# Kernel tuning notes

Hardware: AMD Instinct MI355X
Metric: run time of the kernel (lower is better)

Reference implementation:

```python
import jax, jax.numpy as jnp
import numpy as np

EPS = 1e-07
N, Q = 1368, 21
WS = [16, 32, 64]
ST = [4, 8, 16]
OC = [64, 128, 256]


def _num_pos(n, w, s):
    return int((n - w) / s - EPS) + 1


def setup_inputs() -> dict:
    key = jax.random.key(0)
    kx, k0, k1, k2 = jax.random.split(key, 4)
    B = 64
    x = jax.random.normal(kx, (B, Q, N), dtype=jnp.float32)
    ws = []
    for kk, (w, s, d) in zip([k0, k1, k2], zip(WS, ST, OC)):
        P = _num_pos(N, w, s)
        # xavier-style small init, shape (Nk, q*w) as in FilterbankLinear.weight
        scale = np.sqrt(2.0 / (Q * w + d)).astype(np.float32)
        ws.append(scale * jax.random.normal(kk, (d * P, Q * w), dtype=jnp.float32))
    return {"x": x, "w0": ws[0], "w1": ws[1], "w2": ws[2]}


def _filterbank_linear(x, W, w, s, d):
    # x: (B, q, N); W: (d*P, q*w)
    B, q, n = x.shape
    P = _num_pos(n, w, s)
    # window starts: j*s for j in range(P-1), last window anchored at n-w
    starts = np.concatenate([np.arange(P - 1) * s, np.array([n - w])])
    idx = starts[:, None] + np.arange(w)            # (P, w) static gather indices
    win = x[:, :, idx]                              # (B, q, P, w)
    win = jnp.transpose(win, (0, 2, 1, 3)).reshape(B, P, q * w)  # (B, P, q*w), channel-major like fbank
    h = jnp.einsum('bpf,pdf->bpd', win, W.reshape(P, d, q * w))
    return h.reshape(B, P * d)


def reference(x, w0, w1, w2):
    # FilterbankEdge.forward(x, sample=False): concat of each FilterbankLinear output
    outs = [
        _filterbank_linear(x, W, w, s, d)
        for W, (w, s, d) in zip([w0, w1, w2], zip(WS, ST, OC))
    ]
    return jnp.concatenate(outs, axis=-1)  # (B, 64000)
```

## Files before the change

### kernel.cpp

```cpp
#include <hip/hip_runtime.h>

#define QDIM 21
#define NDIM 1368
#define QN (QDIM * NDIM)
#define OUTSTRIDE 64000
#define XTOT (64 * QN)

typedef __attribute__((ext_vector_type(4))) float f32x4;
typedef __attribute__((ext_vector_type(8))) short bf16x8s;
typedef __attribute__((ext_vector_type(4))) unsigned int u32x4;

typedef __attribute__((address_space(1))) const unsigned int* gas_p;
typedef __attribute__((address_space(3))) unsigned int* las_p;

static __device__ __forceinline__ void gload16(const void* g, char* l) {
    __builtin_amdgcn_global_load_lds((gas_p)g, (las_p)(void*)l, 16, 0, 0);
}

static __device__ __forceinline__ unsigned int pk2(float lo, float hi) {
    unsigned int a = __float_as_uint(lo) + 0x8000u;
    unsigned int b = __float_as_uint(hi) + 0x8000u;
    return __builtin_amdgcn_perm(b, a, 0x07060302);
}

static __device__ __forceinline__ bf16x8s pack8(f32x4 lo, f32x4 hi) {
    u32x4 p;
    p[0] = pk2(lo[0], lo[1]);
    p[1] = pk2(lo[2], lo[3]);
    p[2] = pk2(hi[0], hi[1]);
    p[3] = pk2(hi[2], hi[3]);
    return __builtin_bit_cast(bf16x8s, p);
}

static __device__ __forceinline__ int chunk_swz(int idx, int n) {
    int xcd = idx & 7;
    int i   = idx >> 3;
    int q = n >> 3, r = n & 7;
    int base = (xcd < r) ? xcd * (q + 1) : r * (q + 1) + (xcd - r) * q;
    return base + i;
}

__global__ __launch_bounds__(256)
void xcvt(const float* __restrict__ x, unsigned short* __restrict__ xb) {
    int i = (blockIdx.x * 256 + threadIdx.x) * 8;
    if (i >= XTOT) return;
    f32x4 lo = *(const f32x4*)(x + i);
    f32x4 hi = *(const f32x4*)(x + i + 4);
    *(u32x4*)(xb + i) = __builtin_bit_cast(u32x4, pack8(lo, hi));
}

template<int WLOG2, int NTX, int D, int P, int S, int K, bool ABF16>
__device__ __forceinline__ void fbk_body(const float* __restrict__ x,
                                         const unsigned short* __restrict__ xb,
                                         const float* __restrict__ W,
                                         float* __restrict__ out, int bid,
                                         char* ldsraw) {
    constexpr int WWIN = 1 << WLOG2;
    constexpr int G = (K + 31) / 32;
    constexpr bool TAIL = (K % 32) != 0;
    constexpr int KREM = K & 31;
    constexpr int FMAXC = (K - 4) & ~3;
    constexpr int ASTB = ABF16 ? 4096 : 8192;
    constexpr int STB  = ASTB + 8192;

    const int n0 = (bid % NTX) * 64;
    const int p  = bid / NTX;
    const int start = (p == P - 1) ? (NDIM - WWIN) : p * S;

    const int tid  = threadIdx.x;
    const int wid  = tid >> 6;
    const int lane = tid & 63;
    const int wm = (wid >> 1) * 32;
    const int wn = (wid & 1) * 32;
    const int lr = lane & 15;
    const int hi = lane >> 4;
    const int kb = hi * 8;

    const int lrow = lane >> 3;
    const int g4   = ((lane & 7) ^ lrow) * 4;
    const float* Wp  = W + (size_t)(p * D + n0) * K;
    const float* wb0 = Wp + (size_t)(16 * wid + lrow) * K;
    const float* wb1 = wb0 + (size_t)8 * K;
    const int wB = 2048 * wid;

    const unsigned short* xr0 = xb + (size_t)(16 * wid + (lane >> 2)) * QN + start;
    const float* xf0 = x + (size_t)(16 * wid + lrow) * QN + start;

    auto STAGE = [&](int t, int sbase) {
        if constexpr (ABF16) {
            int fa = t * 32 + (lane & 3) * 8;
            if constexpr (TAIL) fa = (fa > K - 8) ? (K - 8) : fa;
            int qa = fa >> WLOG2, ja = fa & (WWIN - 1);
            gload16(xr0 + qa * NDIM + ja, ldsraw + sbase + 1024 * wid);
        } else {
            int fa = t * 32 + g4;
            if constexpr (TAIL) fa = (fa > FMAXC) ? FMAXC : fa;
            int qa = fa >> WLOG2, ja = fa & (WWIN - 1);
            const float* ga = xf0 + qa * NDIM + ja;
            char* la = ldsraw + sbase + 2048 * wid;
            gload16(ga, la);
            gload16(ga + (size_t)8 * QN, la + 1024);
        }
        int f = t * 32 + g4;
        if constexpr (TAIL) f = (f > FMAXC) ? FMAXC : f;
        char* lb = ldsraw + sbase + ASTB + wB;
        gload16(wb0 + f, lb);
        gload16(wb1 + f, lb + 1024);
    };

    const int x7 = lr & 7;
    const int c0 = ((hi * 2)     ^ x7) * 16;
    const int c1 = ((hi * 2 + 1) ^ x7) * 16;
    const int oA0b = (wm + lr) * 64 + hi * 16;
    const int oA1b = oA0b + 1024;
    const int oA0f = (wm + lr) * 128;
    const int oA1f = (wm + 16 + lr) * 128;
    const int oB0 = ASTB + (wn + lr) * 128;
    const int oB1 = ASTB + (wn + 16 + lr) * 128;

    f32x4 acc[2][2] = {};

    STAGE(0, 0);
    STAGE(1, STB);

    int cs = 0;
    #pragma unroll 1
    for (int t = 0; t < G; ++t) {
        if (t + 1 < G) {
            if constexpr (ABF16) asm volatile("s_waitcnt vmcnt(3)" ::: "memory");
            else                 asm volatile("s_waitcnt vmcnt(4)" ::: "memory");
        } else {
            asm volatile("s_waitcnt vmcnt(0)" ::: "memory");
        }
        __builtin_amdgcn_sched_barrier(0);
        __builtin_amdgcn_s_barrier();
        __builtin_amdgcn_sched_barrier(0);

        const char* sb = ldsraw + cs;
        bf16x8s A0, A1;
        if constexpr (ABF16) {
            A0 = *(const bf16x8s*)(sb + oA0b);
            A1 = *(const bf16x8s*)(sb + oA1b);
            if constexpr (TAIL) {
                if (t == G - 1 && kb >= KREM) {
                    A0 = __builtin_bit_cast(bf16x8s, (u32x4){0u, 0u, 0u, 0u});
                    A1 = A0;
                }
            }
        } else {
            f32x4 a00 = *(const f32x4*)(sb + oA0f + c0);
            f32x4 a01 = *(const f32x4*)(sb + oA0f + c1);
            f32x4 a10 = *(const f32x4*)(sb + oA1f + c0);
            f32x4 a11 = *(const f32x4*)(sb + oA1f + c1);
            if constexpr (TAIL) {
                if (t == G - 1 && kb >= KREM) {
                    f32x4 z = {0.f, 0.f, 0.f, 0.f};
                    a00 = z; a01 = z; a10 = z; a11 = z;
                }
            }
            A0 = pack8(a00, a01);
            A1 = pack8(a10, a11);
        }
        f32x4 b00 = *(const f32x4*)(sb + oB0 + c0);
        f32x4 b01 = *(const f32x4*)(sb + oB0 + c1);
        f32x4 b10 = *(const f32x4*)(sb + oB1 + c0);
        f32x4 b11 = *(const f32x4*)(sb + oB1 + c1);
        bf16x8s B0 = pack8(b00, b01);
        bf16x8s B1 = pack8(b10, b11);

        acc[0][0] = __builtin_amdgcn_mfma_f32_16x16x32_bf16(A0, B0, acc[0][0], 0, 0, 0);
        acc[0][1] = __builtin_amdgcn_mfma_f32_16x16x32_bf16(A0, B1, acc[0][1], 0, 0, 0);
        acc[1][0] = __builtin_amdgcn_mfma_f32_16x16x32_bf16(A1, B0, acc[1][0], 0, 0, 0);
        acc[1][1] = __builtin_amdgcn_mfma_f32_16x16x32_bf16(A1, B1, acc[1][1], 0, 0, 0);

        __builtin_amdgcn_sched_barrier(0);
        if (t + 2 < G) {
            int pb = (cs == 0) ? 2 * STB : cs - STB;
            STAGE(t + 2, pb);
        }
        cs = (cs == 2 * STB) ? 0 : cs + STB;
    }

    const int colbase = p * D + n0;
    #pragma unroll
    for (int mi = 0; mi < 2; ++mi) {
        #pragma unroll
        for (int ni = 0; ni < 2; ++ni) {
            int col = colbase + wn + ni * 16 + lr;
            int rbase = wm + mi * 16 + hi * 4;
            #pragma unroll
            for (int r = 0; r < 4; ++r) {
                out[(size_t)(rbase + r) * OUTSTRIDE + col] = acc[mi][ni][r];
            }
        }
    }
}

template<bool BF>
__global__ __launch_bounds__(256, 4)
void fbk_fused(const float* __restrict__ x,  const unsigned short* __restrict__ xb,
               const float* __restrict__ w0, const float* __restrict__ w1,
               const float* __restrict__ w2, float* __restrict__ out) {
    constexpr int STB = BF ? 12288 : 16384;
    __shared__ __align__(16) char ldsraw[3 * STB];
    const int pb = blockIdx.x;
    if (pb < 328) {
        fbk_body<6, 4, 256, 82, 16, 1344, BF>(x, xb, w2, out + 43008, chunk_swz(pb, 328), ldsraw);
    } else if (pb < 662) {
        fbk_body<5, 2, 128, 167, 8, 672, BF>(x, xb, w1, out + 21632, chunk_swz(pb - 328, 334), ldsraw);
    } else {
        fbk_body<4, 1, 64, 338, 4, 336, BF>(x, xb, w0, out, chunk_swz(pb - 662, 338), ldsraw);
    }
}

extern "C" void kernel_launch(void* const* d_in, const int* in_sizes, int n_in,
                              void* d_out, int out_size, void* d_ws, size_t ws_size,
                              hipStream_t stream) {
    const float* x  = (const float*)d_in[0];
    const float* w0 = (const float*)d_in[1];
    const float* w1 = (const float*)d_in[2];
    const float* w2 = (const float*)d_in[3];
    float* out = (float*)d_out;
    constexpr size_t XBF_BYTES = (size_t)XTOT * 2;
    if (ws_size >= XBF_BYTES) {
        unsigned short* xbuf = (unsigned short*)d_ws;
        xcvt<<<dim3((XTOT / 8 + 255) / 256), 256, 0, stream>>>(x, xbuf);
        fbk_fused<true><<<dim3(1000), 256, 0, stream>>>(x, xbuf, w0, w1, w2, out);
    } else {
        fbk_fused<false><<<dim3(1000), 256, 0, stream>>>(x, nullptr, w0, w1, w2, out);
    }
}
```

Before: 45.34 us.

## Double K-step to 64 with double-buffered LDS, drop fp32 fallback path

The GEMM main loop now consumes 64 K elements per stage instead of 32, doing two MFMA k-steps per barrier. It switches from a three-stage prefetch-ahead-by-two ring to a two-buffer scheme that issues the next stage right after the barrier and then waits for vmcnt(0) each iteration. The goal is to halve the barrier and loop overhead per unit of work. In exchange, LDS per block grows, launch bounds drop to 3 blocks per CU, and prefetch depth is shallower. The fp32-activation fallback is removed, so the workspace is now always assumed large enough for the bf16 copy of x.

```diff
diff --git a/kernel.cpp b/kernel.cpp
--- a/kernel.cpp
+++ b/kernel.cpp
@@ -49,19 +49,16 @@
     *(u32x4*)(xb + i) = __builtin_bit_cast(u32x4, pack8(lo, hi));
 }
 
-template<int WLOG2, int NTX, int D, int P, int S, int K, bool ABF16>
-__device__ __forceinline__ void fbk_body(const float* __restrict__ x,
-                                         const unsigned short* __restrict__ xb,
+template<int WLOG2, int NTX, int D, int P, int S, int K>
+__device__ __forceinline__ void fbk_body(const unsigned short* __restrict__ xb,
                                          const float* __restrict__ W,
                                          float* __restrict__ out, int bid,
-                                         char* ldsraw) {
+                                         char* lds) {
     constexpr int WWIN = 1 << WLOG2;
-    constexpr int G = (K + 31) / 32;
-    constexpr bool TAIL = (K % 32) != 0;
-    constexpr int KREM = K & 31;
-    constexpr int FMAXC = (K - 4) & ~3;
-    constexpr int ASTB = ABF16 ? 4096 : 8192;
-    constexpr int STB  = ASTB + 8192;
+    constexpr int G = (K + 63) / 64;
+    constexpr bool TAIL = (K % 64) != 0;
+    constexpr int KREM = K % 64;
+    constexpr int STB = 24576;
 
     const int n0 = (bid % NTX) * 64;
     const int p  = bid / NTX;
@@ -76,109 +73,83 @@
     const int hi = lane >> 4;
     const int kb = hi * 8;
 
-    const int lrow = lane >> 3;
-    const int g4   = ((lane & 7) ^ lrow) * 4;
-    const float* Wp  = W + (size_t)(p * D + n0) * K;
-    const float* wb0 = Wp + (size_t)(16 * wid + lrow) * K;
-    const float* wb1 = wb0 + (size_t)8 * K;
-    const int wB = 2048 * wid;
+    const int ar   = lane >> 3;
+    const int aseg = ((lane & 7) ^ ar) * 8;
+    const unsigned short* xrA = xb + (size_t)(16 * wid + ar) * QN + start;
 
-    const unsigned short* xr0 = xb + (size_t)(16 * wid + (lane >> 2)) * QN + start;
-    const float* xf0 = x + (size_t)(16 * wid + lrow) * QN + start;
+    const int br = lane >> 4;
+    const float* wbase = W + (size_t)(p * D + n0 + 16 * wid) * K;
 
     auto STAGE = [&](int t, int sbase) {
-        if constexpr (ABF16) {
-            int fa = t * 32 + (lane & 3) * 8;
+        {
+            int fa = t * 64 + aseg;
             if constexpr (TAIL) fa = (fa > K - 8) ? (K - 8) : fa;
-            int qa = fa >> WLOG2, ja = fa & (WWIN - 1);
-            gload16(xr0 + qa * NDIM + ja, ldsraw + sbase + 1024 * wid);
-        } else {
-            int fa = t * 32 + g4;
-            if constexpr (TAIL) fa = (fa > FMAXC) ? FMAXC : fa;
-            int qa = fa >> WLOG2, ja = fa & (WWIN - 1);
-            const float* ga = xf0 + qa * NDIM + ja;
-            char* la = ldsraw + sbase + 2048 * wid;
+            int q = fa >> WLOG2, j = fa & (WWIN - 1);
+            const unsigned short* ga = xrA + q * NDIM + j;
+            char* la = lds + sbase + wid * 2048;
             gload16(ga, la);
             gload16(ga + (size_t)8 * QN, la + 1024);
         }
-        int f = t * 32 + g4;
-        if constexpr (TAIL) f = (f > FMAXC) ? FMAXC : f;
-        char* lb = ldsraw + sbase + ASTB + wB;
-        gload16(wb0 + f, lb);
-        gload16(wb1 + f, lb + 1024);
+        #pragma unroll
+        for (int g = 0; g < 4; ++g) {
+            int srow = 4 * g + br;
+            int scol = ((lane & 15) ^ srow) * 4;
+            int fb = t * 64 + scol;
+            if constexpr (TAIL) fb = (fb > K - 4) ? (K - 4) : fb;
+            gload16(wbase + (size_t)srow * K + fb,
+                    lds + sbase + 8192 + wid * 4096 + g * 1024);
+        }
     };
 
-    const int x7 = lr & 7;
-    const int c0 = ((hi * 2)     ^ x7) * 16;
-    const int c1 = ((hi * 2 + 1) ^ x7) * 16;
-    const int oA0b = (wm + lr) * 64 + hi * 16;
-    const int oA1b = oA0b + 1024;
-    const int oA0f = (wm + lr) * 128;
-    const int oA1f = (wm + 16 + lr) * 128;
-    const int oB0 = ASTB + (wn + lr) * 128;
-    const int oB1 = ASTB + (wn + 16 + lr) * 128;
+    const int oA0 = (wm + lr) * 128;
+    const int oA1 = oA0 + 2048;
+    const int oB0 = 8192 + (wn + lr) * 256;
+    const int oB1 = oB0 + 4096;
+    int cA[2], cB[2][2];
+    #pragma unroll
+    for (int kk = 0; kk < 2; ++kk) {
+        cA[kk]    = ((kk * 4 + hi) ^ (lr & 7)) * 16;
+        cB[kk][0] = ((kk * 8 + hi * 2)     ^ lr) * 16;
+        cB[kk][1] = ((kk * 8 + hi * 2 + 1) ^ lr) * 16;
+    }
 
     f32x4 acc[2][2] = {};
 
     STAGE(0, 0);
-    STAGE(1, STB);
 
-    int cs = 0;
     #pragma unroll 1
     for (int t = 0; t < G; ++t) {
-        if (t + 1 < G) {
-            if constexpr (ABF16) asm volatile("s_waitcnt vmcnt(3)" ::: "memory");
-            else                 asm volatile("s_waitcnt vmcnt(4)" ::: "memory");
-        } else {
-            asm volatile("s_waitcnt vmcnt(0)" ::: "memory");
-        }
+        asm volatile("s_waitcnt vmcnt(0)" ::: "memory");
         __builtin_amdgcn_sched_barrier(0);
         __builtin_amdgcn_s_barrier();
         __builtin_amdgcn_sched_barrier(0);
 
-        const char* sb = ldsraw + cs;
-        bf16x8s A0, A1;
-        if constexpr (ABF16) {
-            A0 = *(const bf16x8s*)(sb + oA0b);
-            A1 = *(const bf16x8s*)(sb + oA1b);
+        if (t + 1 < G) STAGE(t + 1, (t & 1) ? 0 : STB);
+        __builtin_amdgcn_sched_barrier(0);
+
+        const char* sb = lds + ((t & 1) ? STB : 0);
+        #pragma unroll
+        for (int kk = 0; kk < 2; ++kk) {
+            bf16x8s A0 = *(const bf16x8s*)(sb + oA0 + cA[kk]);
+            bf16x8s A1 = *(const bf16x8s*)(sb + oA1 + cA[kk]);
             if constexpr (TAIL) {
-                if (t == G - 1 && kb >= KREM) {
+                if (t == G - 1 && kk * 32 + kb >= KREM) {
                     A0 = __builtin_bit_cast(bf16x8s, (u32x4){0u, 0u, 0u, 0u});
                     A1 = A0;
                 }
             }
-        } else {
-            f32x4 a00 = *(const f32x4*)(sb + oA0f + c0);
-            f32x4 a01 = *(const f32x4*)(sb + oA0f + c1);
-            f32x4 a10 = *(const f32x4*)(sb + oA1f + c0);
-            f32x4 a11 = *(const f32x4*)(sb + oA1f + c1);
-            if constexpr (TAIL) {
-                if (t == G - 1 && kb >= KREM) {
-                    f32x4 z = {0.f, 0.f, 0.f, 0.f};
-                    a00 = z; a01 = z; a10 = z; a11 = z;
-                }
-            }
-            A0 = pack8(a00, a01);
-            A1 = pack8(a10, a11);
+            f32x4 b00 = *(const f32x4*)(sb + oB0 + cB[kk][0]);
+            f32x4 b01 = *(const f32x4*)(sb + oB0 + cB[kk][1]);
+            f32x4 b10 = *(const f32x4*)(sb + oB1 + cB[kk][0]);
+            f32x4 b11 = *(const f32x4*)(sb + oB1 + cB[kk][1]);
+            bf16x8s B0 = pack8(b00, b01);
+            bf16x8s B1 = pack8(b10, b11);
+
+            acc[0][0] = __builtin_amdgcn_mfma_f32_16x16x32_bf16(A0, B0, acc[0][0], 0, 0, 0);
+            acc[0][1] = __builtin_amdgcn_mfma_f32_16x16x32_bf16(A0, B1, acc[0][1], 0, 0, 0);
+            acc[1][0] = __builtin_amdgcn_mfma_f32_16x16x32_bf16(A1, B0, acc[1][0], 0, 0, 0);
+            acc[1][1] = __builtin_amdgcn_mfma_f32_16x16x32_bf16(A1, B1, acc[1][1], 0, 0, 0);
         }
-        f32x4 b00 = *(const f32x4*)(sb + oB0 + c0);
-        f32x4 b01 = *(const f32x4*)(sb + oB0 + c1);
-        f32x4 b10 = *(const f32x4*)(sb + oB1 + c0);
-        f32x4 b11 = *(const f32x4*)(sb + oB1 + c1);
-        bf16x8s B0 = pack8(b00, b01);
-        bf16x8s B1 = pack8(b10, b11);
-
-        acc[0][0] = __builtin_amdgcn_mfma_f32_16x16x32_bf16(A0, B0, acc[0][0], 0, 0, 0);
-        acc[0][1] = __builtin_amdgcn_mfma_f32_16x16x32_bf16(A0, B1, acc[0][1], 0, 0, 0);
-        acc[1][0] = __builtin_amdgcn_mfma_f32_16x16x32_bf16(A1, B0, acc[1][0], 0, 0, 0);
-        acc[1][1] = __builtin_amdgcn_mfma_f32_16x16x32_bf16(A1, B1, acc[1][1], 0, 0, 0);
-
-        __builtin_amdgcn_sched_barrier(0);
-        if (t + 2 < G) {
-            int pb = (cs == 0) ? 2 * STB : cs - STB;
-            STAGE(t + 2, pb);
-        }
-        cs = (cs == 2 * STB) ? 0 : cs + STB;
     }
 
     const int colbase = p * D + n0;
@@ -196,20 +167,18 @@
     }
 }
 
-template<bool BF>
-__global__ __launch_bounds__(256, 4)
-void fbk_fused(const float* __restrict__ x,  const unsigned short* __restrict__ xb,
+__global__ __launch_bounds__(256, 3)
+void fbk_fused(const unsigned short* __restrict__ xb,
                const float* __restrict__ w0, const float* __restrict__ w1,
                const float* __restrict__ w2, float* __restrict__ out) {
-    constexpr int STB = BF ? 12288 : 16384;
-    __shared__ __align__(16) char ldsraw[3 * STB];
+    __shared__ __align__(16) char lds[2 * 24576];
     const int pb = blockIdx.x;
     if (pb < 328) {
-        fbk_body<6, 4, 256, 82, 16, 1344, BF>(x, xb, w2, out + 43008, chunk_swz(pb, 328), ldsraw);
+        fbk_body<6, 4, 256, 82, 16, 1344>(xb, w2, out + 43008, chunk_swz(pb, 328), lds);
     } else if (pb < 662) {
-        fbk_body<5, 2, 128, 167, 8, 672, BF>(x, xb, w1, out + 21632, chunk_swz(pb - 328, 334), ldsraw);
+        fbk_body<5, 2, 128, 167, 8, 672>(xb, w1, out + 21632, chunk_swz(pb - 328, 334), lds);
     } else {
-        fbk_body<4, 1, 64, 338, 4, 336, BF>(x, xb, w0, out, chunk_swz(pb - 662, 338), ldsraw);
+        fbk_body<4, 1, 64, 338, 4, 336>(xb, w0, out, chunk_swz(pb - 662, 338), lds);
     }
 }
 
@@ -221,12 +190,7 @@
     const float* w1 = (const float*)d_in[2];
     const float* w2 = (const float*)d_in[3];
     float* out = (float*)d_out;
-    constexpr size_t XBF_BYTES = (size_t)XTOT * 2;
-    if (ws_size >= XBF_BYTES) {
-        unsigned short* xbuf = (unsigned short*)d_ws;
-        xcvt<<<dim3((XTOT / 8 + 255) / 256), 256, 0, stream>>>(x, xbuf);
-        fbk_fused<true><<<dim3(1000), 256, 0, stream>>>(x, xbuf, w0, w1, w2, out);
-    } else {
-        fbk_fused<false><<<dim3(1000), 256, 0, stream>>>(x, nullptr, w0, w1, w2, out);
-    }
+    unsigned short* xbuf = (unsigned short*)d_ws;
+    xcvt<<<dim3((XTOT / 8 + 255) / 256), 256, 0, stream>>>(x, xbuf);
+    fbk_fused<<<dim3(1000), 256, 0, stream>>>(xbuf, w0, w1, w2, out);
 }
```

Result: faster. 44.36 us (-2.2%).
